# Performance work log

Hardware: AMD Instinct MI355X
Metric: run time of the kernel (lower is better)

## Reference

```python
import jax, jax.numpy as jnp
import numpy as np

N_NODES = 100000
N_EDGES = 3200000
N_GRAPHS = 512
IN_CH = 128
HID = 32
OUT = 2


def setup_inputs() -> dict:
    key = jax.random.key(0)
    ks = jax.random.split(key, 6)
    x = jax.random.normal(ks[0], (N_NODES, IN_CH), dtype=jnp.float32)
    edge_index = jax.random.randint(ks[1], (2, N_EDGES), 0, N_NODES, dtype=jnp.int64)
    batch = jnp.sort(jax.random.randint(ks[2], (N_NODES,), 0, N_GRAPHS, dtype=jnp.int64))
    # Glorot-ish params
    W1 = jax.random.normal(ks[3], (IN_CH, HID), dtype=jnp.float32) * (1.0 / np.sqrt(IN_CH))
    b1 = jnp.zeros((HID,), dtype=jnp.float32)
    W2 = jax.random.normal(ks[4], (HID, HID), dtype=jnp.float32) * (1.0 / np.sqrt(HID))
    b2 = jnp.zeros((HID,), dtype=jnp.float32)
    Wl = jax.random.normal(ks[5], (HID, OUT), dtype=jnp.float32) * (1.0 / np.sqrt(HID))
    bl = jnp.zeros((OUT,), dtype=jnp.float32)
    return {"x": x, "edge_index": edge_index, "batch": batch,
            "W1": W1, "b1": b1, "W2": W2, "b2": b2, "Wl": Wl, "bl": bl}


def _gcn_conv(h, src, dst, W, b, n_nodes):
    # PyG GCNConv: transform, add self-loops, symmetric deg normalization,
    # scatter-add messages from src -> dst, then bias.
    h = h @ W  # [N, F_out]
    ones = jnp.ones(src.shape[0], dtype=h.dtype)
    # degree on target nodes, +1 for the implicit self-loop
    deg = jax.ops.segment_sum(ones, dst, num_segments=n_nodes) + 1.0
    dinv = jax.lax.rsqrt(deg)  # deg >= 1 always
    norm = dinv[src] * dinv[dst]  # [E]
    agg = jax.ops.segment_sum(h[src] * norm[:, None], dst, num_segments=n_nodes)
    # self-loop contribution: norm_ii = dinv_i^2
    agg = agg + h * (dinv * dinv)[:, None]
    return agg + b


def reference(x, edge_index, batch, W1, b1, W2, b2, Wl, bl):
    n_nodes = x.shape[0]
    src, dst = edge_index[0], edge_index[1]
    h = jax.nn.relu(_gcn_conv(x, src, dst, W1, b1, n_nodes))
    h = jax.nn.relu(_gcn_conv(h, src, dst, W2, b2, n_nodes))
    # global mean pool per graph
    sums = jax.ops.segment_sum(h, batch, num_segments=N_GRAPHS)
    counts = jax.ops.segment_sum(jnp.ones(n_nodes, h.dtype), batch, num_segments=N_GRAPHS)
    pooled = sums / jnp.maximum(counts, 1.0)[:, None]  # [G, 32]
    return pooled @ Wl + bl  # [G, 2]
```

## Files before the change

### kernel.cpp

```cpp
#include <hip/hip_runtime.h>
#include <hip/hip_bf16.h>

#define N_NODES 100000
#define N_EDGES 3200000
#define N_GRAPHS 512
#define NBUK 782
#define CAP 4608
#define FILL_CHUNK 8192
#define FILL_BLOCKS ((N_EDGES + FILL_CHUNK - 1) / FILL_CHUNK)

__device__ __forceinline__ float blo(unsigned v) { return __uint_as_float(v << 16); }
__device__ __forceinline__ float bhi(unsigned v) { return __uint_as_float(v & 0xffff0000u); }

__global__ __launch_bounds__(1024) void k_binfill(const int* __restrict__ ei,
                                                  int* __restrict__ gcnt,
                                                  unsigned* __restrict__ packed) {
    __shared__ int h[NBUK];
    __shared__ int base[NBUK];
    __shared__ int sb[NBUK];
    __shared__ int sc[1024];
    __shared__ unsigned buf[FILL_CHUNK] __attribute__((aligned(16)));
    int t = threadIdx.x;
    for (int i = t; i < NBUK; i += 1024) h[i] = 0;
    __syncthreads();
    int s0 = blockIdx.x * FILL_CHUNK;
    int ng = min(FILL_CHUNK, N_EDGES - s0) >> 2;
    const int4* src4 = (const int4*)(ei + s0);
    const int4* dst4 = (const int4*)(ei + N_EDGES + s0);
    int4 sv[2], dv[2];
    int  rk[2][4];
#pragma unroll
    for (int g = 0; g < 2; g++) {
        int gi = t + g * 1024;
        if (gi < ng) {
            sv[g] = src4[gi];
            dv[g] = dst4[gi];
            rk[g][0] = atomicAdd(&h[dv[g].x >> 7], 1);
            rk[g][1] = atomicAdd(&h[dv[g].y >> 7], 1);
            rk[g][2] = atomicAdd(&h[dv[g].z >> 7], 1);
            rk[g][3] = atomicAdd(&h[dv[g].w >> 7], 1);
        }
    }
    __syncthreads();
    for (int i = t; i < NBUK; i += 1024) {
        int c = h[i];
        base[i] = c ? atomicAdd(&gcnt[i], c) : 0;
    }
    sc[t] = (t < NBUK) ? h[t] : 0;
    __syncthreads();
    for (int off = 1; off < 1024; off <<= 1) {
        int x = (t >= off) ? sc[t - off] : 0;
        __syncthreads();
        sc[t] += x;
        __syncthreads();
    }
    for (int i = t; i < NBUK; i += 1024) sb[i] = sc[i] - h[i];
    __syncthreads();
#pragma unroll
    for (int g = 0; g < 2; g++) {
        int gi = t + g * 1024;
        if (gi < ng) {
            int s[4] = {sv[g].x, sv[g].y, sv[g].z, sv[g].w};
            int d[4] = {dv[g].x, dv[g].y, dv[g].z, dv[g].w};
#pragma unroll
            for (int k = 0; k < 4; k++) {
                int bk = d[k] >> 7;
                buf[sb[bk] + rk[g][k]] = (unsigned)s[k] | (((unsigned)d[k] & 127u) << 17);
            }
        }
    }
    __syncthreads();
    int w = t >> 6, lane = t & 63;
    for (int bk = w; bk < NBUK; bk += 16) {
        int c = h[bk];
        if (!c) continue;
        unsigned* gp = packed + (size_t)bk * CAP + base[bk];
        int lb = sb[bk];
        for (int j = lane; j < c; j += 64) gp[j] = buf[lb + j];
    }
}

__global__ __launch_bounds__(512) void k_csr(const unsigned* __restrict__ packed,
                                             const int* __restrict__ gcnt,
                                             int* __restrict__ rp, int* __restrict__ rpe,
                                             float* __restrict__ dinv,
                                             int* __restrict__ csr) {
    __shared__ int deg[128];
    __shared__ int sd[128];
    __shared__ int nb0[128];
    __shared__ int lcsr[CAP] __attribute__((aligned(16)));
    int t = threadIdx.x;
    int b = blockIdx.x;
    if (t < 128) deg[t] = 0;
    __syncthreads();
    int n = gcnt[b];
    const unsigned* pb = packed + (size_t)b * CAP;
    unsigned pv[3][4];
    int rk[3][4];
#pragma unroll
    for (int g = 0; g < 3; g++) {
        int i0 = 4 * (t + g * 512);
        if (i0 < n) {
            if (i0 + 3 < n) {
                uint4 p = *(const uint4*)(pb + i0);
                pv[g][0] = p.x; pv[g][1] = p.y; pv[g][2] = p.z; pv[g][3] = p.w;
            } else {
#pragma unroll
                for (int k = 0; k < 4; k++) pv[g][k] = (i0 + k < n) ? pb[i0 + k] : 0u;
            }
#pragma unroll
            for (int k = 0; k < 4; k++)
                if (i0 + k < n) rk[g][k] = atomicAdd(&deg[pv[g][k] >> 17], 1);
        }
    }
    __syncthreads();
    int d = (t < 128) ? deg[t] : 0;
    if (t < 128) sd[t] = d;
    __syncthreads();
    for (int off = 1; off < 128; off <<= 1) {
        int x = (t >= off && t < 128) ? sd[t - off] : 0;
        __syncthreads();
        if (t < 128) sd[t] += x;
        __syncthreads();
    }
    if (t < 128) {
        int l0 = sd[t] - d;
        nb0[t] = l0;
        int node = b * 128 + t;
        if (node < N_NODES) {
            rp[node] = b * CAP + l0;
            rpe[node] = b * CAP + l0 + d;
            dinv[node] = rsqrtf((float)d + 1.0f);
        }
    }
    __syncthreads();
#pragma unroll
    for (int g = 0; g < 3; g++) {
        int i0 = 4 * (t + g * 512);
        if (i0 < n) {
#pragma unroll
            for (int k = 0; k < 4; k++) {
                if (i0 + k < n) {
                    unsigned p = pv[g][k];
                    lcsr[nb0[p >> 17] + rk[g][k]] = (int)(p & 0x1FFFFu);
                }
            }
        }
    }
    __syncthreads();
    int n4 = (n + 3) >> 2;
    int4* dst4 = (int4*)(csr + (size_t)b * CAP);
    const int4* sl4 = (const int4*)lcsr;
    for (int i = t; i < n4; i += 512) dst4[i] = sl4[i];
}

__global__ void k_gemm1(const float* __restrict__ x, const float* __restrict__ W1,
                        const float* __restrict__ dinv, __hip_bfloat16* __restrict__ H1s) {
    __shared__ float Ws[128 * 32];
    __shared__ float xs[32 * 128];
    int t = threadIdx.x;
    const float4* W4 = (const float4*)W1;
    float4* Ws4 = (float4*)Ws;
#pragma unroll
    for (int i = 0; i < 4; i++) Ws4[t + 256 * i] = W4[t + 256 * i];
    int row0 = blockIdx.x * 32;
    const float4* x4 = (const float4*)(x + (size_t)row0 * 128);
    float4* xs4 = (float4*)xs;
#pragma unroll
    for (int i = 0; i < 4; i++) xs4[t + 256 * i] = x4[t + 256 * i];
    __syncthreads();
    int col = t & 31;
    int rb = (t >> 5) * 4;
    float a0 = 0.f, a1 = 0.f, a2 = 0.f, a3 = 0.f;
#pragma unroll 8
    for (int k = 0; k < 128; k++) {
        float w = Ws[k * 32 + col];
        a0 += xs[(rb + 0) * 128 + k] * w;
        a1 += xs[(rb + 1) * 128 + k] * w;
        a2 += xs[(rb + 2) * 128 + k] * w;
        a3 += xs[(rb + 3) * 128 + k] * w;
    }
    int r = row0 + rb;
    __hip_bfloat16* o = H1s + (size_t)r * 32 + col;
    o[0]  = __float2bfloat16(a0 * dinv[r + 0]);
    o[32] = __float2bfloat16(a1 * dinv[r + 1]);
    o[64] = __float2bfloat16(a2 * dinv[r + 2]);
    o[96] = __float2bfloat16(a3 * dinv[r + 3]);
}

__global__ void k_gemm2(const float* __restrict__ h1, const float* __restrict__ W2,
                        const float* __restrict__ dinv, __hip_bfloat16* __restrict__ H2s) {
    __shared__ float Ws[32 * 32];
    __shared__ float xs[32 * 32];
    int t = threadIdx.x;
    ((float4*)Ws)[t] = ((const float4*)W2)[t];
    int row0 = blockIdx.x * 32;
    ((float4*)xs)[t] = ((const float4*)(h1 + (size_t)row0 * 32))[t];
    __syncthreads();
    int col = t & 31;
    int rb = (t >> 5) * 4;
    float a0 = 0.f, a1 = 0.f, a2 = 0.f, a3 = 0.f;
#pragma unroll
    for (int k = 0; k < 32; k++) {
        float w = Ws[k * 32 + col];
        a0 += xs[(rb + 0) * 32 + k] * w;
        a1 += xs[(rb + 1) * 32 + k] * w;
        a2 += xs[(rb + 2) * 32 + k] * w;
        a3 += xs[(rb + 3) * 32 + k] * w;
    }
    int r = row0 + rb;
    __hip_bfloat16* o = H2s + (size_t)r * 32 + col;
    o[0]  = __float2bfloat16(a0 * dinv[r + 0]);
    o[32] = __float2bfloat16(a1 * dinv[r + 1]);
    o[64] = __float2bfloat16(a2 * dinv[r + 2]);
    o[96] = __float2bfloat16(a3 * dinv[r + 3]);
}

__global__ void k_gather(const __hip_bfloat16* __restrict__ Hs, const float* __restrict__ dinv,
                         const int* __restrict__ rp, const int* __restrict__ rpe,
                         const int* __restrict__ csr,
                         const float* __restrict__ bias, float* __restrict__ hout) {
    int wid = (blockIdx.x * 256 + threadIdx.x) >> 6;
    if (wid >= N_NODES) return;
    const uint4* H4 = (const uint4*)Hs;
    int lane = threadIdx.x & 63;
    int fb = lane & 3;
    int es = lane >> 2;
    int beg = rp[wid];
    int deg = rpe[wid] - beg;
    float a0=0.f,a1=0.f,a2=0.f,a3=0.f,a4=0.f,a5=0.f,a6=0.f,a7=0.f;
    for (int eb = 0; eb < deg; eb += 64) {
        int cv = csr[beg + eb + lane];
#pragma unroll
        for (int k = 0; k < 4; k++) {
            int e = eb + es + 16 * k;
            int src = __shfl(cv, es + 16 * k);
            if (e < deg) {
                uint4 v = H4[(size_t)src * 4 + fb];
                a0 += blo(v.x); a1 += bhi(v.x);
                a2 += blo(v.y); a3 += bhi(v.y);
                a4 += blo(v.z); a5 += bhi(v.z);
                a6 += blo(v.w); a7 += bhi(v.w);
            }
        }
    }
#pragma unroll
    for (int m = 4; m <= 32; m <<= 1) {
        a0 += __shfl_xor(a0, m); a1 += __shfl_xor(a1, m);
        a2 += __shfl_xor(a2, m); a3 += __shfl_xor(a3, m);
        a4 += __shfl_xor(a4, m); a5 += __shfl_xor(a5, m);
        a6 += __shfl_xor(a6, m); a7 += __shfl_xor(a7, m);
    }
    if (es == 0) {
        float di = dinv[wid];
        uint4 vw = H4[(size_t)wid * 4 + fb];
        float4 bA = *(const float4*)(bias + fb * 8);
        float4 bB = *(const float4*)(bias + fb * 8 + 4);
        float4 oA, oB;
        oA.x = fmaxf((a0 + blo(vw.x)) * di + bA.x, 0.f);
        oA.y = fmaxf((a1 + bhi(vw.x)) * di + bA.y, 0.f);
        oA.z = fmaxf((a2 + blo(vw.y)) * di + bA.z, 0.f);
        oA.w = fmaxf((a3 + bhi(vw.y)) * di + bA.w, 0.f);
        oB.x = fmaxf((a4 + blo(vw.z)) * di + bB.x, 0.f);
        oB.y = fmaxf((a5 + bhi(vw.z)) * di + bB.y, 0.f);
        oB.z = fmaxf((a6 + blo(vw.w)) * di + bB.z, 0.f);
        oB.w = fmaxf((a7 + bhi(vw.w)) * di + bB.w, 0.f);
        float* o = hout + (size_t)wid * 32 + fb * 8;
        *(float4*)o = oA;
        *(float4*)(o + 4) = oB;
    }
}

__global__ __launch_bounds__(256) void k_pool(const float* __restrict__ h2,
                                              const int* __restrict__ batch,
                                              const float* __restrict__ Wl,
                                              const float* __restrict__ bl,
                                              float* __restrict__ out) {
    __shared__ float red[256];
    __shared__ float pooled[32];
    int g = blockIdx.x;
    int t = threadIdx.x;
    int lo = 0, hi = N_NODES;
    while (lo < hi) { int m = (lo + hi) >> 1; if (batch[m] < g) lo = m + 1; else hi = m; }
    int s = lo;
    hi = N_NODES;
    while (lo < hi) { int m = (lo + hi) >> 1; if (batch[m] < g + 1) lo = m + 1; else hi = m; }
    int e = lo;
    int f = t & 31, r0 = t >> 5;
    float acc = 0.f;
    for (int r = s + r0; r < e; r += 8) acc += h2[(size_t)r * 32 + f];
    red[t] = acc;
    __syncthreads();
    for (int off = 128; off >= 32; off >>= 1) {
        if (t < off) red[t] += red[t + off];
        __syncthreads();
    }
    if (t < 32) pooled[t] = red[t] / fmaxf((float)(e - s), 1.0f);
    __syncthreads();
    if (t < 2) {
        float a = bl[t];
#pragma unroll
        for (int k = 0; k < 32; k++) a += pooled[k] * Wl[k * 2 + t];
        out[g * 2 + t] = a;
    }
}

extern "C" void kernel_launch(void* const* d_in, const int* in_sizes, int n_in,
                              void* d_out, int out_size, void* d_ws, size_t ws_size,
                              hipStream_t stream) {
    const float* x    = (const float*)d_in[0];
    const int*   ei   = (const int*)d_in[1];
    const int*   batch= (const int*)d_in[2];
    const float* W1   = (const float*)d_in[3];
    const float* b1   = (const float*)d_in[4];
    const float* W2   = (const float*)d_in[5];
    const float* b2   = (const float*)d_in[6];
    const float* Wl   = (const float*)d_in[7];
    const float* bl   = (const float*)d_in[8];
    float* out = (float*)d_out;

    char* w = (char*)d_ws;
    size_t off = 0;
    auto take = [&](size_t bytes) -> char* {
        char* p = w + off;
        off = (off + bytes + 255) & ~(size_t)255;
        return p;
    };
    __hip_bfloat16* H1s = (__hip_bfloat16*)take((size_t)N_NODES * 32 * 2);
    float*          h1  = (float*)take((size_t)N_NODES * 32 * 4);
    char*           shared = take((size_t)NBUK * CAP * 4);
    unsigned*       packed = (unsigned*)shared;
    __hip_bfloat16* H2s    = (__hip_bfloat16*)shared;
    int*      csr    = (int*)  take((size_t)NBUK * CAP * 4 + 1024);
    float*    dinv   = (float*)take((size_t)N_NODES * 4);
    int*      rp     = (int*)  take((size_t)N_NODES * 4);
    int*      rpe    = (int*)  take((size_t)N_NODES * 4);
    int*      gcnt   = (int*)  take((size_t)NBUK * 4);

    hipMemsetAsync(gcnt, 0, (size_t)NBUK * 4, stream);

    k_binfill<<<FILL_BLOCKS, 1024, 0, stream>>>(ei, gcnt, packed);
    k_csr    <<<NBUK, 512, 0, stream>>>(packed, gcnt, rp, rpe, dinv, csr);
    k_gemm1  <<<N_NODES / 32, 256, 0, stream>>>(x, W1, dinv, H1s);
    k_gather <<<N_NODES / 4, 256, 0, stream>>>(H1s, dinv, rp, rpe, csr, b1, h1);
    k_gemm2  <<<N_NODES / 32, 256, 0, stream>>>(h1, W2, dinv, H2s);
    k_gather <<<N_NODES / 4, 256, 0, stream>>>(H2s, dinv, rp, rpe, csr, b2, h1);
    k_pool   <<<N_GRAPHS, 256, 0, stream>>>(h1, batch, Wl, bl, out);
}
```

Measured before the change: 289.9 us.

## Use global per-node degree atomics for CSR ranks and fuse GEMM2 into first gather

The binning kernel now also does a global atomicAdd per destination node. Each edge gets a rank within its node, packed into the top bits of the edge word. The CSR kernel then takes degrees from that global array and scatters edges directly, dropping its shared-memory histogram pass. Separately, the layer-1 gather now applies bias and ReLU and multiplies by W2 in shared memory, which removes the fp32 h1 round-trip and the separate gemm2 launch. This costs 3.2M global atomics and an extra memset, and ranks above 255 would overflow the 8-bit rank field.

```diff
diff --git a/kernel.cpp b/kernel.cpp
--- a/kernel.cpp
+++ b/kernel.cpp
@@ -14,6 +14,7 @@
 
 __global__ __launch_bounds__(1024) void k_binfill(const int* __restrict__ ei,
                                                   int* __restrict__ gcnt,
+                                                  int* __restrict__ gdeg,
                                                   unsigned* __restrict__ packed) {
     __shared__ int h[NBUK];
     __shared__ int base[NBUK];
@@ -29,6 +30,7 @@
     const int4* dst4 = (const int4*)(ei + N_EDGES + s0);
     int4 sv[2], dv[2];
     int  rk[2][4];
+    int  rg[2][4];
 #pragma unroll
     for (int g = 0; g < 2; g++) {
         int gi = t + g * 1024;
@@ -39,6 +41,10 @@
             rk[g][1] = atomicAdd(&h[dv[g].y >> 7], 1);
             rk[g][2] = atomicAdd(&h[dv[g].z >> 7], 1);
             rk[g][3] = atomicAdd(&h[dv[g].w >> 7], 1);
+            rg[g][0] = atomicAdd(&gdeg[dv[g].x], 1);
+            rg[g][1] = atomicAdd(&gdeg[dv[g].y], 1);
+            rg[g][2] = atomicAdd(&gdeg[dv[g].z], 1);
+            rg[g][3] = atomicAdd(&gdeg[dv[g].w], 1);
         }
     }
     __syncthreads();
@@ -65,7 +71,9 @@
 #pragma unroll
             for (int k = 0; k < 4; k++) {
                 int bk = d[k] >> 7;
-                buf[sb[bk] + rk[g][k]] = (unsigned)s[k] | (((unsigned)d[k] & 127u) << 17);
+                buf[sb[bk] + rk[g][k]] = (unsigned)s[k]
+                                       | (((unsigned)d[k] & 127u) << 17)
+                                       | ((unsigned)rg[g][k] << 24);
             }
         }
     }
@@ -82,40 +90,21 @@
 
 __global__ __launch_bounds__(512) void k_csr(const unsigned* __restrict__ packed,
                                              const int* __restrict__ gcnt,
+                                             const int* __restrict__ gdeg,
                                              int* __restrict__ rp, int* __restrict__ rpe,
                                              float* __restrict__ dinv,
                                              int* __restrict__ csr) {
-    __shared__ int deg[128];
     __shared__ int sd[128];
     __shared__ int nb0[128];
     __shared__ int lcsr[CAP] __attribute__((aligned(16)));
     int t = threadIdx.x;
     int b = blockIdx.x;
-    if (t < 128) deg[t] = 0;
-    __syncthreads();
-    int n = gcnt[b];
-    const unsigned* pb = packed + (size_t)b * CAP;
-    unsigned pv[3][4];
-    int rk[3][4];
-#pragma unroll
-    for (int g = 0; g < 3; g++) {
-        int i0 = 4 * (t + g * 512);
-        if (i0 < n) {
-            if (i0 + 3 < n) {
-                uint4 p = *(const uint4*)(pb + i0);
-                pv[g][0] = p.x; pv[g][1] = p.y; pv[g][2] = p.z; pv[g][3] = p.w;
-            } else {
-#pragma unroll
-                for (int k = 0; k < 4; k++) pv[g][k] = (i0 + k < n) ? pb[i0 + k] : 0u;
-            }
-#pragma unroll
-            for (int k = 0; k < 4; k++)
-                if (i0 + k < n) rk[g][k] = atomicAdd(&deg[pv[g][k] >> 17], 1);
-        }
-    }
-    __syncthreads();
-    int d = (t < 128) ? deg[t] : 0;
-    if (t < 128) sd[t] = d;
+    int d = 0;
+    if (t < 128) {
+        int node = b * 128 + t;
+        d = (node < N_NODES) ? gdeg[node] : 0;
+        sd[t] = d;
+    }
     __syncthreads();
     for (int off = 1; off < 128; off <<= 1) {
         int x = (t >= off && t < 128) ? sd[t - off] : 0;
@@ -134,24 +123,26 @@
         }
     }
     __syncthreads();
-#pragma unroll
-    for (int g = 0; g < 3; g++) {
-        int i0 = 4 * (t + g * 512);
-        if (i0 < n) {
-#pragma unroll
-            for (int k = 0; k < 4; k++) {
-                if (i0 + k < n) {
-                    unsigned p = pv[g][k];
-                    lcsr[nb0[p >> 17] + rk[g][k]] = (int)(p & 0x1FFFFu);
-                }
-            }
-        }
-    }
-    __syncthreads();
-    int n4 = (n + 3) >> 2;
+    int n = gcnt[b];
+    const unsigned* pb = packed + (size_t)b * CAP;
+    int n4 = n >> 2;
+    const uint4* pb4 = (const uint4*)pb;
+    for (int i = t; i < n4; i += 512) {
+        uint4 p = pb4[i];
+        lcsr[nb0[(p.x >> 17) & 127u] + (p.x >> 24)] = (int)(p.x & 0x1FFFFu);
+        lcsr[nb0[(p.y >> 17) & 127u] + (p.y >> 24)] = (int)(p.y & 0x1FFFFu);
+        lcsr[nb0[(p.z >> 17) & 127u] + (p.z >> 24)] = (int)(p.z & 0x1FFFFu);
+        lcsr[nb0[(p.w >> 17) & 127u] + (p.w >> 24)] = (int)(p.w & 0x1FFFFu);
+    }
+    for (int i = (n4 << 2) + t; i < n; i += 512) {
+        unsigned p = pb[i];
+        lcsr[nb0[(p >> 17) & 127u] + (p >> 24)] = (int)(p & 0x1FFFFu);
+    }
+    __syncthreads();
+    int nq = (n + 3) >> 2;
     int4* dst4 = (int4*)(csr + (size_t)b * CAP);
     const int4* sl4 = (const int4*)lcsr;
-    for (int i = t; i < n4; i += 512) dst4[i] = sl4[i];
+    for (int i = t; i < nq; i += 512) dst4[i] = sl4[i];
 }
 
 __global__ void k_gemm1(const float* __restrict__ x, const float* __restrict__ W1,
@@ -188,32 +179,75 @@
     o[96] = __float2bfloat16(a3 * dinv[r + 3]);
 }
 
-__global__ void k_gemm2(const float* __restrict__ h1, const float* __restrict__ W2,
-                        const float* __restrict__ dinv, __hip_bfloat16* __restrict__ H2s) {
-    __shared__ float Ws[32 * 32];
-    __shared__ float xs[32 * 32];
-    int t = threadIdx.x;
-    ((float4*)Ws)[t] = ((const float4*)W2)[t];
-    int row0 = blockIdx.x * 32;
-    ((float4*)xs)[t] = ((const float4*)(h1 + (size_t)row0 * 32))[t];
-    __syncthreads();
-    int col = t & 31;
-    int rb = (t >> 5) * 4;
-    float a0 = 0.f, a1 = 0.f, a2 = 0.f, a3 = 0.f;
-#pragma unroll
-    for (int k = 0; k < 32; k++) {
-        float w = Ws[k * 32 + col];
-        a0 += xs[(rb + 0) * 32 + k] * w;
-        a1 += xs[(rb + 1) * 32 + k] * w;
-        a2 += xs[(rb + 2) * 32 + k] * w;
-        a3 += xs[(rb + 3) * 32 + k] * w;
-    }
-    int r = row0 + rb;
-    __hip_bfloat16* o = H2s + (size_t)r * 32 + col;
-    o[0]  = __float2bfloat16(a0 * dinv[r + 0]);
-    o[32] = __float2bfloat16(a1 * dinv[r + 1]);
-    o[64] = __float2bfloat16(a2 * dinv[r + 2]);
-    o[96] = __float2bfloat16(a3 * dinv[r + 3]);
+__global__ __launch_bounds__(256) void k_gather1f(const __hip_bfloat16* __restrict__ Hs,
+                                                  const float* __restrict__ dinv,
+                                                  const int* __restrict__ rp,
+                                                  const int* __restrict__ rpe,
+                                                  const int* __restrict__ csr,
+                                                  const float* __restrict__ bias,
+                                                  const float* __restrict__ W2,
+                                                  __hip_bfloat16* __restrict__ H2s) {
+    __shared__ float W2s[32 * 32];
+    __shared__ float rows[4][32];
+    int t = threadIdx.x;
+    ((float4*)W2s)[t] = ((const float4*)W2)[t];
+    int wid = (blockIdx.x * 256 + t) >> 6;
+    const uint4* H4 = (const uint4*)Hs;
+    int lane = t & 63;
+    int fb = lane & 3;
+    int es = lane >> 2;
+    int beg = rp[wid];
+    int deg = rpe[wid] - beg;
+    float a0=0.f,a1=0.f,a2=0.f,a3=0.f,a4=0.f,a5=0.f,a6=0.f,a7=0.f;
+    for (int eb = 0; eb < deg; eb += 64) {
+        int cv = csr[beg + eb + lane];
+#pragma unroll
+        for (int k = 0; k < 4; k++) {
+            int e = eb + es + 16 * k;
+            int src = __shfl(cv, es + 16 * k);
+            if (e < deg) {
+                uint4 v = H4[(size_t)src * 4 + fb];
+                a0 += blo(v.x); a1 += bhi(v.x);
+                a2 += blo(v.y); a3 += bhi(v.y);
+                a4 += blo(v.z); a5 += bhi(v.z);
+                a6 += blo(v.w); a7 += bhi(v.w);
+            }
+        }
+    }
+#pragma unroll
+    for (int m = 4; m <= 32; m <<= 1) {
+        a0 += __shfl_xor(a0, m); a1 += __shfl_xor(a1, m);
+        a2 += __shfl_xor(a2, m); a3 += __shfl_xor(a3, m);
+        a4 += __shfl_xor(a4, m); a5 += __shfl_xor(a5, m);
+        a6 += __shfl_xor(a6, m); a7 += __shfl_xor(a7, m);
+    }
+    int w = t >> 6;
+    if (es == 0) {
+        float di = dinv[wid];
+        uint4 vw = H4[(size_t)wid * 4 + fb];
+        float4 bA = *(const float4*)(bias + fb * 8);
+        float4 bB = *(const float4*)(bias + fb * 8 + 4);
+        float4 oA, oB;
+        oA.x = fmaxf((a0 + blo(vw.x)) * di + bA.x, 0.f);
+        oA.y = fmaxf((a1 + bhi(vw.x)) * di + bA.y, 0.f);
+        oA.z = fmaxf((a2 + blo(vw.y)) * di + bA.z, 0.f);
+        oA.w = fmaxf((a3 + bhi(vw.y)) * di + bA.w, 0.f);
+        oB.x = fmaxf((a4 + blo(vw.z)) * di + bB.x, 0.f);
+        oB.y = fmaxf((a5 + bhi(vw.z)) * di + bB.y, 0.f);
+        oB.z = fmaxf((a6 + blo(vw.w)) * di + bB.z, 0.f);
+        oB.w = fmaxf((a7 + bhi(vw.w)) * di + bB.w, 0.f);
+        *(float4*)&rows[w][fb * 8] = oA;
+        *(float4*)&rows[w][fb * 8 + 4] = oB;
+    }
+    __syncthreads();
+    if (lane < 32) {
+        int node = blockIdx.x * 4 + w;
+        float di = dinv[node];
+        float acc = 0.f;
+#pragma unroll
+        for (int k = 0; k < 32; k++) acc += rows[w][k] * W2s[k * 32 + lane];
+        H2s[(size_t)node * 32 + lane] = __float2bfloat16(acc * di);
+    }
 }
 
 __global__ void k_gather(const __hip_bfloat16* __restrict__ Hs, const float* __restrict__ dinv,
@@ -336,14 +370,15 @@
     int*      rp     = (int*)  take((size_t)N_NODES * 4);
     int*      rpe    = (int*)  take((size_t)N_NODES * 4);
     int*      gcnt   = (int*)  take((size_t)NBUK * 4);
+    int*      gdeg   = (int*)  take((size_t)N_NODES * 4);
 
     hipMemsetAsync(gcnt, 0, (size_t)NBUK * 4, stream);
-
-    k_binfill<<<FILL_BLOCKS, 1024, 0, stream>>>(ei, gcnt, packed);
-    k_csr    <<<NBUK, 512, 0, stream>>>(packed, gcnt, rp, rpe, dinv, csr);
-    k_gemm1  <<<N_NODES / 32, 256, 0, stream>>>(x, W1, dinv, H1s);
-    k_gather <<<N_NODES / 4, 256, 0, stream>>>(H1s, dinv, rp, rpe, csr, b1, h1);
-    k_gemm2  <<<N_NODES / 32, 256, 0, stream>>>(h1, W2, dinv, H2s);
-    k_gather <<<N_NODES / 4, 256, 0, stream>>>(H2s, dinv, rp, rpe, csr, b2, h1);
-    k_pool   <<<N_GRAPHS, 256, 0, stream>>>(h1, batch, Wl, bl, out);
-}
+    hipMemsetAsync(gdeg, 0, (size_t)N_NODES * 4, stream);
+
+    k_binfill <<<FILL_BLOCKS, 1024, 0, stream>>>(ei, gcnt, gdeg, packed);
+    k_csr     <<<NBUK, 512, 0, stream>>>(packed, gcnt, gdeg, rp, rpe, dinv, csr);
+    k_gemm1   <<<N_NODES / 32, 256, 0, stream>>>(x, W1, dinv, H1s);
+    k_gather1f<<<N_NODES / 4, 256, 0, stream>>>(H1s, dinv, rp, rpe, csr, b1, W2, H2s);
+    k_gather  <<<N_NODES / 4, 256, 0, stream>>>(H2s, dinv, rp, rpe, csr, b2, h1);
+    k_pool    <<<N_GRAPHS, 256, 0, stream>>>(h1, batch, Wl, bl, out);
+}
```

Result: slower. 415.7 us (+43.4%).
